# Performance work log

Hardware: AMD Instinct MI355X
Metric: run time of the kernel (lower is better)

The kernel has to match this reference:

```python
import jax, jax.numpy as jnp
import numpy as np

T = 5
EPS = 1e-05
G = 4      # num_groups
D = 64     # num_channels per group


def setup_inputs() -> dict:
    key = jax.random.key(0)
    X = jax.random.normal(key, (32, 256, 56, 56), dtype=jnp.float32)
    weight = jnp.ones((1, 256, 1, 1), dtype=jnp.float32)
    bias = jnp.zeros((1, 256, 1, 1), dtype=jnp.float32)
    return {"X": X, "weight": weight, "bias": bias}


def reference(X, weight, bias):
    N, C, H, W = X.shape
    # (N,C,H,W) -> (C,N,H,W) -> (g, d, m) with m = N*H*W
    x = X.transpose(1, 0, 2, 3).reshape(G, D, -1)
    m = x.shape[-1]
    mean = x.mean(-1, keepdims=True)                 # (g, d, 1)
    xc = x - mean
    I = jnp.eye(D, dtype=X.dtype)
    # Sigma = eps*I + xc xc^T / m     (g, d, d)
    Sigma = EPS * I + jnp.einsum('gdm,gem->gde', xc, xc) / m
    # trace normalization
    rTr = 1.0 / jnp.trace(Sigma, axis1=1, axis2=2)[:, None, None]  # (g,1,1)
    Sn = Sigma * rTr
    # Newton-Schulz iterations: P_{k+1} = 1.5 P_k - 0.5 P_k^3 Sn
    P = jnp.broadcast_to(I, (G, D, D))
    for _ in range(T):
        P = 1.5 * P - 0.5 * (P @ P @ P @ Sn)
    wm = P * jnp.sqrt(rTr)                           # whitening matrix (g,d,d)
    xn = wm @ xc                                     # (g, d, m)
    Xh = xn.reshape(C, N, H, W).transpose(1, 0, 2, 3)
    return Xh * weight + bias
```

## Files before the change

kernel.cpp:

```cpp
#include <hip/hip_runtime.h>
#include <math.h>

#define GROUPS 4
#define DCH    64
#define NBATCH 32
#define CTOT   256
#define HW     3136
#define CHW    (CTOT*HW)
#define MTOT   (NBATCH*HW)
#define EPSV   1e-5f

typedef __attribute__((ext_vector_type(8))) short bf16x8;
typedef __attribute__((ext_vector_type(4))) float f32x4;

__device__ __forceinline__ f32x4 mfma16(bf16x8 a, bf16x8 b, f32x4 c) {
    return __builtin_amdgcn_mfma_f32_16x16x32_bf16(a, b, c, 0, 0, 0);
}

__device__ __forceinline__ void split2(float x, short& h, short& l) {
    union { float f; unsigned u; } c; c.f = x;
    h = (short)(c.u >> 16);
    union { unsigned u; float f; } hm; hm.u = c.u & 0xFFFF0000u;
    union { float f; unsigned u; } lo; lo.f = x - hm.f;
    l = (short)(lo.u >> 16);
}

__device__ __forceinline__ void load_slab(const float* bp, float dst[16]) {
    float4 a0 = *reinterpret_cast<const float4*>(bp);
    float4 a1 = *reinterpret_cast<const float4*>(bp + 4);
    float4 b0 = *reinterpret_cast<const float4*>(bp + 32);
    float4 b1 = *reinterpret_cast<const float4*>(bp + 36);
    dst[0]=a0.x; dst[1]=a0.y; dst[2]=a0.z;  dst[3]=a0.w;
    dst[4]=a1.x; dst[5]=a1.y; dst[6]=a1.z;  dst[7]=a1.w;
    dst[8]=b0.x; dst[9]=b0.y; dst[10]=b0.z; dst[11]=b0.w;
    dst[12]=b1.x; dst[13]=b1.y; dst[14]=b1.z; dst[15]=b1.w;
}

template <int TPB>
__global__ __launch_bounds__(512) void k1_gram(const float* __restrict__ X,
                                               float* __restrict__ pGram,
                                               float* __restrict__ pSum)
{
    constexpr int KPB = MTOT / TPB;
    constexpr int NST = KPB / 128;
    const int pb   = blockIdx.x;
    const int g    = blockIdx.y;
    const int tid  = threadIdx.x;
    const int w    = tid >> 6;
    const int lane = tid & 63;
    const int tr   = w & 3;
    const int par  = w >> 2;
    const int lr   = lane & 15;
    const int q    = lane >> 4;

    __shared__ float smem[8192];
    __shared__ float rsum[2][64];

    f32x4 acc[4];
#pragma unroll
    for (int c = 0; c < 4; ++c) acc[c] = (f32x4)(0.f);
    float sumv = 0.f;

    const float* Xg  = X + (size_t)g * DCH * HW;
    const int    row = 16 * tr + lr;

    float xv[2][16];
    {
        const int kk = pb * KPB + par * 64;
        const int n  = kk / HW;
        const int s  = kk - n * HW;
        load_slab(Xg + (size_t)n * CHW + (size_t)row * HW + s + q * 8, xv[0]);
    }

#pragma unroll
    for (int t = 0; t < NST; ++t) {
        if (t + 1 < NST) {
            const int kk = pb * KPB + (t + 1) * 128 + par * 64;
            const int n  = kk / HW;
            const int s  = kk - n * HW;
            load_slab(Xg + (size_t)n * CHW + (size_t)row * HW + s + q * 8,
                      xv[(t + 1) & 1]);
        }
        bf16x8 ah[2], al[2];
#pragma unroll
        for (int ks = 0; ks < 2; ++ks) {
#pragma unroll
            for (int j = 0; j < 8; ++j) {
                float x = xv[t & 1][ks * 8 + j];
                sumv += x;
                short h, l; split2(x, h, l);
                ah[ks][j] = h; al[ks][j] = l;
            }
        }
#pragma unroll
        for (int ks = 0; ks < 2; ++ks) {
            *reinterpret_cast<bf16x8*>(&smem[(((par*4+tr)*2+ks)*2+0)*256 + lane*4]) = ah[ks];
            *reinterpret_cast<bf16x8*>(&smem[(((par*4+tr)*2+ks)*2+1)*256 + lane*4]) = al[ks];
        }
        __syncthreads();
#pragma unroll
        for (int c = 0; c < 4; ++c) {
#pragma unroll
            for (int ks = 0; ks < 2; ++ks) {
                bf16x8 bh = *reinterpret_cast<const bf16x8*>(
                    &smem[(((par*4+c)*2+ks)*2+0)*256 + lane*4]);
                bf16x8 bl = *reinterpret_cast<const bf16x8*>(
                    &smem[(((par*4+c)*2+ks)*2+1)*256 + lane*4]);
                acc[c] = mfma16(ah[ks], bh, acc[c]);
                acc[c] = mfma16(ah[ks], bl, acc[c]);
                acc[c] = mfma16(al[ks], bh, acc[c]);
            }
        }
        __syncthreads();
    }

    sumv += __shfl_xor(sumv, 16);
    sumv += __shfl_xor(sumv, 32);
    if (q == 0) rsum[par][row] = sumv;

#pragma unroll
    for (int c = 0; c < 4; ++c) {
#pragma unroll
        for (int r = 0; r < 4; ++r) {
            smem[par * 4096 + (16 * tr + 4 * q + r) * 64 + 16 * c + lr] = acc[c][r];
        }
    }
    __syncthreads();

    float* pg = pGram + ((size_t)g * TPB + pb) * 4096;
    for (int i = tid; i < 4096; i += 512) pg[i] = smem[i] + smem[4096 + i];
    if (tid < 64)
        pSum[((size_t)g * TPB + pb) * 64 + tid] = rsum[0][tid] + rsum[1][tid];
}

template <int S, int SLICE>
__global__ __launch_bounds__(256) void k2a1(const float* __restrict__ pGram,
                                            const float* __restrict__ pSum,
                                            float* __restrict__ pG2,
                                            float* __restrict__ pS2)
{
    const int cb  = blockIdx.x;
    const int g   = blockIdx.y;
    const int s   = blockIdx.z;
    const int tid = threadIdx.x;
    const int e = tid & 63, q = tid >> 6;
    __shared__ float red[4][64];
    __shared__ float red2[4][64];

    const float* pg = pGram + ((size_t)g * (S * SLICE) + s * SLICE + q) * 4096 + cb * 64 + e;
    float sum = 0.f;
#pragma unroll
    for (int i = 0; i < SLICE / 4; ++i)
        sum += pg[(size_t)i * 4 * 4096];
    red[q][e] = sum;
    if (cb == 0) {
        const float* ps = pSum + ((size_t)g * (S * SLICE) + s * SLICE + q) * 64 + e;
        float s2 = 0.f;
#pragma unroll
        for (int i = 0; i < SLICE / 4; ++i)
            s2 += ps[i * 4 * 64];
        red2[q][e] = s2;
    }
    __syncthreads();
    if (tid < 64) {
        pG2[((size_t)g * S + s) * 4096 + cb * 64 + tid] =
            red[0][tid] + red[1][tid] + red[2][tid] + red[3][tid];
        if (cb == 0)
            pS2[((size_t)g * S + s) * 64 + tid] =
                red2[0][tid] + red2[1][tid] + red2[2][tid] + red2[3][tid];
    }
}

template <int S>
__global__ __launch_bounds__(256) void k2a2(const float* __restrict__ pG2,
                                            const float* __restrict__ pS2,
                                            float* __restrict__ Gram,
                                            float* __restrict__ Mean)
{
    const int bx  = blockIdx.x;
    const int g   = blockIdx.y;
    const int tid = threadIdx.x;
    const int idx = bx * 256 + tid;

    float sum = 0.f;
#pragma unroll
    for (int s = 0; s < S; ++s)
        sum += pG2[((size_t)g * S + s) * 4096 + idx];
    Gram[g * 4096 + idx] = sum;

    if (bx == 0 && tid < 64) {
        float s2 = 0.f;
#pragma unroll
        for (int s = 0; s < S; ++s)
            s2 += pS2[((size_t)g * S + s) * 64 + tid];
        Mean[g * 64 + tid] = s2 * (1.0f / (float)MTOT);
    }
}

__device__ __forceinline__ void packrow2(const float* __restrict__ M, int row, int q,
                                         bf16x8& h0, bf16x8& l0,
                                         bf16x8& h1, bf16x8& l1)
{
    const float* p = M + row * 68 + 8 * q;
    float4 a0 = *reinterpret_cast<const float4*>(p);
    float4 a1 = *reinterpret_cast<const float4*>(p + 4);
    float4 b0 = *reinterpret_cast<const float4*>(p + 32);
    float4 b1 = *reinterpret_cast<const float4*>(p + 36);
    float e0[8] = {a0.x, a0.y, a0.z, a0.w, a1.x, a1.y, a1.z, a1.w};
    float e1[8] = {b0.x, b0.y, b0.z, b0.w, b1.x, b1.y, b1.z, b1.w};
#pragma unroll
    for (int j = 0; j < 8; ++j) {
        short h, l;
        split2(e0[j], h, l); h0[j] = h; l0[j] = l;
        split2(e1[j], h, l); h1[j] = h; l1[j] = l;
    }
}

__device__ __forceinline__ void mm_mfma(const float* __restrict__ A,
                                        const float* __restrict__ B,
                                        int w, int lr, int q, f32x4 acc[4])
{
    bf16x8 ah0, al0, ah1, al1;
    packrow2(A, 16 * w + lr, q, ah0, al0, ah1, al1);
#pragma unroll
    for (int c = 0; c < 4; ++c) {
        bf16x8 bh0, bl0, bh1, bl1;
        packrow2(B, 16 * c + lr, q, bh0, bl0, bh1, bl1);
        acc[c] = mfma16(ah0, bh0, acc[c]);
        acc[c] = mfma16(ah0, bl0, acc[c]);
        acc[c] = mfma16(al0, bh0, acc[c]);
        acc[c] = mfma16(ah1, bh1, acc[c]);
        acc[c] = mfma16(ah1, bl1, acc[c]);
        acc[c] = mfma16(al1, bh1, acc[c]);
    }
}

__global__ __launch_bounds__(256) void k2b_ns(const float* __restrict__ Gram,
                                              const float* __restrict__ Mean,
                                              const float* __restrict__ Wt,
                                              const float* __restrict__ Bs,
                                              float* __restrict__ Aout,
                                              float* __restrict__ Off)
{
    const int g   = blockIdx.x;
    const int tid = threadIdx.x;
    const int w = tid >> 6, lane = tid & 63, lr = lane & 15, q = lane >> 4;
    __shared__ float MP[64 * 68];
    __shared__ float MA[64 * 68];
    __shared__ float MB2[64 * 68];
    __shared__ float MS[64 * 68];
    __shared__ float lmean[64];
    __shared__ float redm[1024];
    __shared__ float rtr_s;

    if (tid < 64) lmean[tid] = Mean[g * 64 + tid];
    __syncthreads();
    for (int idx = tid; idx < 4096; idx += 256) {
        int d = idx >> 6, e = idx & 63;
        float v = Gram[g * 4096 + idx] * (1.0f / (float)MTOT) - lmean[d] * lmean[e];
        if (d == e) v += EPSV;
        MS[d * 68 + e] = v;
        MP[d * 68 + e] = (d == e) ? 1.f : 0.f;
    }
    __syncthreads();
    if (tid < 64) {
        float v = MS[tid * 68 + tid];
#pragma unroll
        for (int off = 32; off > 0; off >>= 1) v += __shfl_down(v, off);
        if (tid == 0) rtr_s = 1.f / v;
    }
    __syncthreads();
    const float rTr = rtr_s;
    for (int idx = tid; idx < 4096; idx += 256) {
        int d = idx >> 6, e = idx & 63;
        MS[d * 68 + e] *= rTr;
    }
    __syncthreads();

    const int row_o = 16 * w + 4 * q;
    for (int it = 0; it < 5; ++it) {
        f32x4 acc[4];
#pragma unroll
        for (int c = 0; c < 4; ++c) acc[c] = (f32x4)(0.f);
        mm_mfma(MP, MP, w, lr, q, acc);
#pragma unroll
        for (int c = 0; c < 4; ++c)
#pragma unroll
            for (int r = 0; r < 4; ++r)
                MA[(row_o + r) * 68 + 16 * c + lr] = acc[c][r];
        __syncthreads();

#pragma unroll
        for (int c = 0; c < 4; ++c) acc[c] = (f32x4)(0.f);
        mm_mfma(MA, MP, w, lr, q, acc);
#pragma unroll
        for (int c = 0; c < 4; ++c)
#pragma unroll
            for (int r = 0; r < 4; ++r)
                MB2[(row_o + r) * 68 + 16 * c + lr] = acc[c][r];
        __syncthreads();

#pragma unroll
        for (int c = 0; c < 4; ++c) acc[c] = (f32x4)(0.f);
        mm_mfma(MB2, MS, w, lr, q, acc);
#pragma unroll
        for (int c = 0; c < 4; ++c)
#pragma unroll
            for (int r = 0; r < 4; ++r) {
                int o = (row_o + r) * 68 + 16 * c + lr;
                MP[o] = 1.5f * MP[o] - 0.5f * acc[c][r];
            }
        __syncthreads();
    }

    const float sc = sqrtf(rTr);
    const int i0 = (tid >> 4) << 2, j0 = (tid & 15) << 2;
#pragma unroll
    for (int i = 0; i < 4; ++i) {
        int d = i0 + i;
        float wv = Wt[g * 64 + d] * sc;
        float4 v;
        v.x = MP[d * 68 + j0 + 0] * wv;
        v.y = MP[d * 68 + j0 + 1] * wv;
        v.z = MP[d * 68 + j0 + 2] * wv;
        v.w = MP[d * 68 + j0 + 3] * wv;
        *reinterpret_cast<float4*>(Aout + g * 4096 + (d << 6) + j0) = v;
        redm[(d << 4) + (tid & 15)] =
            v.x * lmean[j0] + v.y * lmean[j0 + 1] + v.z * lmean[j0 + 2] + v.w * lmean[j0 + 3];
    }
    __syncthreads();
    if (tid < 64) {
        float s = 0.f;
#pragma unroll
        for (int qq = 0; qq < 16; ++qq) s += redm[(tid << 4) + qq];
        Off[g * 64 + tid] = Bs[g * 64 + tid] - s;
    }
}

__global__ __launch_bounds__(256) void k3_apply(const float* __restrict__ X,
                                                const float* __restrict__ Aout,
                                                const float* __restrict__ Off,
                                                float* __restrict__ Y)
{
    const int c    = blockIdx.x;
    const int g    = blockIdx.y;
    const int tid  = threadIdx.x;
    const int w    = tid >> 6;
    const int lane = tid & 63;
    const int lr   = lane & 15;
    const int q    = lane >> 4;

    __shared__ float tile[4096];

    const int col0 = c * 64;
    const int n    = col0 / HW;
    const int s0   = col0 - n * HW;
    const float* Xg   = X + (size_t)g * DCH * HW;
    const float* base = Xg + (size_t)n * CHW + s0;

    float4 xr[4];
#pragma unroll
    for (int k = 0; k < 4; ++k) {
        int f = k * 256 + tid, r = f >> 4, gc = f & 15;
        xr[k] = *reinterpret_cast<const float4*>(base + (size_t)r * HW + gc * 4);
    }

    bf16x8 ah[2], al[2];
#pragma unroll
    for (int s = 0; s < 2; ++s) {
        const float* ap = Aout + g * 4096 + (16 * w + lr) * 64 + 32 * s + 8 * q;
        float4 v0 = *reinterpret_cast<const float4*>(ap);
        float4 v1 = *reinterpret_cast<const float4*>(ap + 4);
        float av[8] = {v0.x, v0.y, v0.z, v0.w, v1.x, v1.y, v1.z, v1.w};
#pragma unroll
        for (int j = 0; j < 8; ++j) {
            short h, l; split2(av[j], h, l);
            ah[s][j] = h; al[s][j] = l;
        }
    }
    float offv[4];
#pragma unroll
    for (int r = 0; r < 4; ++r) offv[r] = Off[g * 64 + 16 * w + 4 * q + r];

#pragma unroll
    for (int k = 0; k < 4; ++k) {
        int f = k * 256 + tid;
        *reinterpret_cast<float4*>(&tile[f * 4]) = xr[k];
    }
    __syncthreads();

    f32x4 accg[4];
#pragma unroll
    for (int j = 0; j < 4; ++j) accg[j] = (f32x4)(0.f);

#pragma unroll
    for (int ks = 0; ks < 2; ++ks) {
        bf16x8 bh[4], bl[4];
#pragma unroll
        for (int j8 = 0; j8 < 8; ++j8) {
            const int row = 32 * ks + 8 * q + j8;
            float4 v = *reinterpret_cast<const float4*>(&tile[row * 64 + lr * 4]);
            float vv[4] = {v.x, v.y, v.z, v.w};
#pragma unroll
            for (int jj = 0; jj < 4; ++jj) {
                short h, l; split2(vv[jj], h, l);
                bh[jj][j8] = h; bl[jj][j8] = l;
            }
        }
#pragma unroll
        for (int jj = 0; jj < 4; ++jj) {
            accg[jj] = mfma16(ah[ks], bh[jj], accg[jj]);
            accg[jj] = mfma16(ah[ks], bl[jj], accg[jj]);
            accg[jj] = mfma16(al[ks], bh[jj], accg[jj]);
        }
    }

    float* yp = Y + (size_t)g * DCH * HW + (size_t)n * CHW + s0 + 4 * lr;
#pragma unroll
    for (int r = 0; r < 4; ++r) {
        int row = 16 * w + 4 * q + r;
        float4 o;
        o.x = accg[0][r] + offv[r];
        o.y = accg[1][r] + offv[r];
        o.z = accg[2][r] + offv[r];
        o.w = accg[3][r] + offv[r];
        *reinterpret_cast<float4*>(yp + (size_t)row * HW) = o;
    }
}

extern "C" void kernel_launch(void* const* d_in, const int* in_sizes, int n_in,
                              void* d_out, int out_size, void* d_ws, size_t ws_size,
                              hipStream_t stream)
{
    const float* X  = (const float*)d_in[0];
    const float* Wt = (const float*)d_in[1];
    const float* Bs = (const float*)d_in[2];
    float* Y  = (float*)d_out;
    float* ws = (float*)d_ws;

    const size_t fixed = (size_t)4 * 4096 + 256 + (size_t)4 * 4096 + 256
                       + (size_t)4 * 7 * 4096 + (size_t)4 * 7 * 64;
    const size_t need392 = ((size_t)4 * 392 * 4096 + (size_t)4 * 392 * 64 + fixed) * sizeof(float);
    const int PBn = (ws_size >= need392) ? 392 : 196;

    float* pGram = ws;
    float* pSum  = pGram + (size_t)4 * PBn * 4096;
    float* Gram  = pSum  + (size_t)4 * PBn * 64;
    float* Mean  = Gram  + 4 * 4096;
    float* Aout  = Mean  + 256;
    float* Off   = Aout  + 4 * 4096;
    float* pG2   = Off   + 256;
    float* pS2   = pG2   + (size_t)4 * 7 * 4096;

    if (PBn == 392) {
        k1_gram<392><<<dim3(392, GROUPS), 512, 0, stream>>>(X, pGram, pSum);
        k2a1<7, 56><<<dim3(64, GROUPS, 7), 256, 0, stream>>>(pGram, pSum, pG2, pS2);
    } else {
        k1_gram<196><<<dim3(196, GROUPS), 512, 0, stream>>>(X, pGram, pSum);
        k2a1<7, 28><<<dim3(64, GROUPS, 7), 256, 0, stream>>>(pGram, pSum, pG2, pS2);
    }
    k2a2<7>   <<<dim3(16, GROUPS), 256, 0, stream>>>(pG2, pS2, Gram, Mean);
    k2b_ns    <<<dim3(GROUPS), 256, 0, stream>>>(Gram, Mean, Wt, Bs, Aout, Off);
    k3_apply  <<<dim3(1568, GROUPS), 256, 0, stream>>>(X, Aout, Off, Y);
}
```

Measured before the change: 85.73 us.

## Fuse final Gram reduction into NS kernel and shorten Newton-Schulz chain

Removes the separate final-reduction kernel by having the Newton-Schulz kernel sum the seven partial Gram/mean slices itself. Starts Newton-Schulz from the closed-form first iterate and computes P^2 and P*Sn in one phase, so each of the four remaining iterations needs two barrier phases instead of three. Also fixes the partial block count at 196, dropping the larger 392-block path, which halves k1's grid and may reduce its parallelism.

```diff
diff --git a/kernel.cpp b/kernel.cpp
--- a/kernel.cpp
+++ b/kernel.cpp
@@ -8,6 +8,7 @@
 #define HW     3136
 #define CHW    (CTOT*HW)
 #define MTOT   (NBATCH*HW)
+#define PB     196
 #define EPSV   1e-5f
 
 typedef __attribute__((ext_vector_type(8))) short bf16x8;
@@ -36,12 +37,11 @@
     dst[12]=b1.x; dst[13]=b1.y; dst[14]=b1.z; dst[15]=b1.w;
 }
 
-template <int TPB>
 __global__ __launch_bounds__(512) void k1_gram(const float* __restrict__ X,
                                                float* __restrict__ pGram,
                                                float* __restrict__ pSum)
 {
-    constexpr int KPB = MTOT / TPB;
+    constexpr int KPB = MTOT / PB;
     constexpr int NST = KPB / 128;
     const int pb   = blockIdx.x;
     const int g    = blockIdx.y;
@@ -127,18 +127,18 @@
     }
     __syncthreads();
 
-    float* pg = pGram + ((size_t)g * TPB + pb) * 4096;
+    float* pg = pGram + ((size_t)g * PB + pb) * 4096;
     for (int i = tid; i < 4096; i += 512) pg[i] = smem[i] + smem[4096 + i];
     if (tid < 64)
-        pSum[((size_t)g * TPB + pb) * 64 + tid] = rsum[0][tid] + rsum[1][tid];
-}
-
-template <int S, int SLICE>
+        pSum[((size_t)g * PB + pb) * 64 + tid] = rsum[0][tid] + rsum[1][tid];
+}
+
 __global__ __launch_bounds__(256) void k2a1(const float* __restrict__ pGram,
                                             const float* __restrict__ pSum,
                                             float* __restrict__ pG2,
                                             float* __restrict__ pS2)
 {
+    constexpr int SLICE = PB / 7;
     const int cb  = blockIdx.x;
     const int g   = blockIdx.y;
     const int s   = blockIdx.z;
@@ -147,14 +147,14 @@
     __shared__ float red[4][64];
     __shared__ float red2[4][64];
 
-    const float* pg = pGram + ((size_t)g * (S * SLICE) + s * SLICE + q) * 4096 + cb * 64 + e;
+    const float* pg = pGram + ((size_t)g * PB + s * SLICE + q) * 4096 + cb * 64 + e;
     float sum = 0.f;
 #pragma unroll
     for (int i = 0; i < SLICE / 4; ++i)
         sum += pg[(size_t)i * 4 * 4096];
     red[q][e] = sum;
     if (cb == 0) {
-        const float* ps = pSum + ((size_t)g * (S * SLICE) + s * SLICE + q) * 64 + e;
+        const float* ps = pSum + ((size_t)g * PB + s * SLICE + q) * 64 + e;
         float s2 = 0.f;
 #pragma unroll
         for (int i = 0; i < SLICE / 4; ++i)
@@ -163,37 +163,11 @@
     }
     __syncthreads();
     if (tid < 64) {
-        pG2[((size_t)g * S + s) * 4096 + cb * 64 + tid] =
+        pG2[((size_t)g * 7 + s) * 4096 + cb * 64 + tid] =
             red[0][tid] + red[1][tid] + red[2][tid] + red[3][tid];
         if (cb == 0)
-            pS2[((size_t)g * S + s) * 64 + tid] =
+            pS2[((size_t)g * 7 + s) * 64 + tid] =
                 red2[0][tid] + red2[1][tid] + red2[2][tid] + red2[3][tid];
-    }
-}
-
-template <int S>
-__global__ __launch_bounds__(256) void k2a2(const float* __restrict__ pG2,
-                                            const float* __restrict__ pS2,
-                                            float* __restrict__ Gram,
-                                            float* __restrict__ Mean)
-{
-    const int bx  = blockIdx.x;
-    const int g   = blockIdx.y;
-    const int tid = threadIdx.x;
-    const int idx = bx * 256 + tid;
-
-    float sum = 0.f;
-#pragma unroll
-    for (int s = 0; s < S; ++s)
-        sum += pG2[((size_t)g * S + s) * 4096 + idx];
-    Gram[g * 4096 + idx] = sum;
-
-    if (bx == 0 && tid < 64) {
-        float s2 = 0.f;
-#pragma unroll
-        for (int s = 0; s < S; ++s)
-            s2 += pS2[((size_t)g * S + s) * 64 + tid];
-        Mean[g * 64 + tid] = s2 * (1.0f / (float)MTOT);
     }
 }
 
@@ -216,27 +190,8 @@
     }
 }
 
-__device__ __forceinline__ void mm_mfma(const float* __restrict__ A,
-                                        const float* __restrict__ B,
-                                        int w, int lr, int q, f32x4 acc[4])
-{
-    bf16x8 ah0, al0, ah1, al1;
-    packrow2(A, 16 * w + lr, q, ah0, al0, ah1, al1);
-#pragma unroll
-    for (int c = 0; c < 4; ++c) {
-        bf16x8 bh0, bl0, bh1, bl1;
-        packrow2(B, 16 * c + lr, q, bh0, bl0, bh1, bl1);
-        acc[c] = mfma16(ah0, bh0, acc[c]);
-        acc[c] = mfma16(ah0, bl0, acc[c]);
-        acc[c] = mfma16(al0, bh0, acc[c]);
-        acc[c] = mfma16(ah1, bh1, acc[c]);
-        acc[c] = mfma16(ah1, bl1, acc[c]);
-        acc[c] = mfma16(al1, bh1, acc[c]);
-    }
-}
-
-__global__ __launch_bounds__(256) void k2b_ns(const float* __restrict__ Gram,
-                                              const float* __restrict__ Mean,
+__global__ __launch_bounds__(256) void k2b_ns(const float* __restrict__ pG2,
+                                              const float* __restrict__ pS2,
                                               const float* __restrict__ Wt,
                                               const float* __restrict__ Bs,
                                               float* __restrict__ Aout,
@@ -253,14 +208,21 @@
     __shared__ float redm[1024];
     __shared__ float rtr_s;
 
-    if (tid < 64) lmean[tid] = Mean[g * 64 + tid];
+    if (tid < 64) {
+        float s2 = 0.f;
+#pragma unroll
+        for (int s = 0; s < 7; ++s) s2 += pS2[((size_t)g * 7 + s) * 64 + tid];
+        lmean[tid] = s2 * (1.0f / (float)MTOT);
+    }
     __syncthreads();
     for (int idx = tid; idx < 4096; idx += 256) {
         int d = idx >> 6, e = idx & 63;
-        float v = Gram[g * 4096 + idx] * (1.0f / (float)MTOT) - lmean[d] * lmean[e];
+        float sum = 0.f;
+#pragma unroll
+        for (int s = 0; s < 7; ++s) sum += pG2[((size_t)g * 7 + s) * 4096 + idx];
+        float v = sum * (1.0f / (float)MTOT) - lmean[d] * lmean[e];
         if (d == e) v += EPSV;
         MS[d * 68 + e] = v;
-        MP[d * 68 + e] = (d == e) ? 1.f : 0.f;
     }
     __syncthreads();
     if (tid < 64) {
@@ -273,36 +235,63 @@
     const float rTr = rtr_s;
     for (int idx = tid; idx < 4096; idx += 256) {
         int d = idx >> 6, e = idx & 63;
-        MS[d * 68 + e] *= rTr;
+        float sv = MS[d * 68 + e] * rTr;
+        MS[d * 68 + e] = sv;
+        MP[d * 68 + e] = ((d == e) ? 1.5f : 0.f) - 0.5f * sv;
     }
     __syncthreads();
 
     const int row_o = 16 * w + 4 * q;
-    for (int it = 0; it < 5; ++it) {
+    for (int it = 0; it < 4; ++it) {
+        f32x4 a2[4], aS[4];
+#pragma unroll
+        for (int c = 0; c < 4; ++c) { a2[c] = (f32x4)(0.f); aS[c] = (f32x4)(0.f); }
+        bf16x8 pah0, pal0, pah1, pal1;
+        packrow2(MP, 16 * w + lr, q, pah0, pal0, pah1, pal1);
+#pragma unroll
+        for (int c = 0; c < 4; ++c) {
+            bf16x8 bh0, bl0, bh1, bl1;
+            packrow2(MP, 16 * c + lr, q, bh0, bl0, bh1, bl1);
+            a2[c] = mfma16(pah0, bh0, a2[c]);
+            a2[c] = mfma16(pah0, bl0, a2[c]);
+            a2[c] = mfma16(pal0, bh0, a2[c]);
+            a2[c] = mfma16(pah1, bh1, a2[c]);
+            a2[c] = mfma16(pah1, bl1, a2[c]);
+            a2[c] = mfma16(pal1, bh1, a2[c]);
+            bf16x8 sh0, sl0, sh1, sl1;
+            packrow2(MS, 16 * c + lr, q, sh0, sl0, sh1, sl1);
+            aS[c] = mfma16(pah0, sh0, aS[c]);
+            aS[c] = mfma16(pah0, sl0, aS[c]);
+            aS[c] = mfma16(pal0, sh0, aS[c]);
+            aS[c] = mfma16(pah1, sh1, aS[c]);
+            aS[c] = mfma16(pah1, sl1, aS[c]);
+            aS[c] = mfma16(pal1, sh1, aS[c]);
+        }
+#pragma unroll
+        for (int c = 0; c < 4; ++c)
+#pragma unroll
+            for (int r = 0; r < 4; ++r) {
+                MA [(row_o + r) * 68 + 16 * c + lr] = a2[c][r];
+                MB2[(row_o + r) * 68 + 16 * c + lr] = aS[c][r];
+            }
+        __syncthreads();
+
         f32x4 acc[4];
 #pragma unroll
         for (int c = 0; c < 4; ++c) acc[c] = (f32x4)(0.f);
-        mm_mfma(MP, MP, w, lr, q, acc);
-#pragma unroll
-        for (int c = 0; c < 4; ++c)
-#pragma unroll
-            for (int r = 0; r < 4; ++r)
-                MA[(row_o + r) * 68 + 16 * c + lr] = acc[c][r];
-        __syncthreads();
-
-#pragma unroll
-        for (int c = 0; c < 4; ++c) acc[c] = (f32x4)(0.f);
-        mm_mfma(MA, MP, w, lr, q, acc);
-#pragma unroll
-        for (int c = 0; c < 4; ++c)
-#pragma unroll
-            for (int r = 0; r < 4; ++r)
-                MB2[(row_o + r) * 68 + 16 * c + lr] = acc[c][r];
-        __syncthreads();
-
-#pragma unroll
-        for (int c = 0; c < 4; ++c) acc[c] = (f32x4)(0.f);
-        mm_mfma(MB2, MS, w, lr, q, acc);
+        bf16x8 qah0, qal0, qah1, qal1;
+        packrow2(MA, 16 * w + lr, q, qah0, qal0, qah1, qal1);
+#pragma unroll
+        for (int c = 0; c < 4; ++c) {
+            bf16x8 bh0, bl0, bh1, bl1;
+            packrow2(MB2, 16 * c + lr, q, bh0, bl0, bh1, bl1);
+            acc[c] = mfma16(qah0, bh0, acc[c]);
+            acc[c] = mfma16(qah0, bl0, acc[c]);
+            acc[c] = mfma16(qal0, bh0, acc[c]);
+            acc[c] = mfma16(qah1, bh1, acc[c]);
+            acc[c] = mfma16(qah1, bl1, acc[c]);
+            acc[c] = mfma16(qal1, bh1, acc[c]);
+        }
 #pragma unroll
         for (int c = 0; c < 4; ++c)
 #pragma unroll
@@ -438,28 +427,15 @@
     float* Y  = (float*)d_out;
     float* ws = (float*)d_ws;
 
-    const size_t fixed = (size_t)4 * 4096 + 256 + (size_t)4 * 4096 + 256
-                       + (size_t)4 * 7 * 4096 + (size_t)4 * 7 * 64;
-    const size_t need392 = ((size_t)4 * 392 * 4096 + (size_t)4 * 392 * 64 + fixed) * sizeof(float);
-    const int PBn = (ws_size >= need392) ? 392 : 196;
-
     float* pGram = ws;
-    float* pSum  = pGram + (size_t)4 * PBn * 4096;
-    float* Gram  = pSum  + (size_t)4 * PBn * 64;
-    float* Mean  = Gram  + 4 * 4096;
-    float* Aout  = Mean  + 256;
+    float* pSum  = pGram + (size_t)4 * PB * 4096;
+    float* pG2   = pSum  + (size_t)4 * PB * 64;
+    float* pS2   = pG2   + (size_t)4 * 7 * 4096;
+    float* Aout  = pS2   + (size_t)4 * 7 * 64;
     float* Off   = Aout  + 4 * 4096;
-    float* pG2   = Off   + 256;
-    float* pS2   = pG2   + (size_t)4 * 7 * 4096;
-
-    if (PBn == 392) {
-        k1_gram<392><<<dim3(392, GROUPS), 512, 0, stream>>>(X, pGram, pSum);
-        k2a1<7, 56><<<dim3(64, GROUPS, 7), 256, 0, stream>>>(pGram, pSum, pG2, pS2);
-    } else {
-        k1_gram<196><<<dim3(196, GROUPS), 512, 0, stream>>>(X, pGram, pSum);
-        k2a1<7, 28><<<dim3(64, GROUPS, 7), 256, 0, stream>>>(pGram, pSum, pG2, pS2);
-    }
-    k2a2<7>   <<<dim3(16, GROUPS), 256, 0, stream>>>(pG2, pS2, Gram, Mean);
-    k2b_ns    <<<dim3(GROUPS), 256, 0, stream>>>(Gram, Mean, Wt, Bs, Aout, Off);
-    k3_apply  <<<dim3(1568, GROUPS), 256, 0, stream>>>(X, Aout, Off, Y);
-}
+
+    k1_gram <<<dim3(PB, GROUPS), 512, 0, stream>>>(X, pGram, pSum);
+    k2a1    <<<dim3(64, GROUPS, 7), 256, 0, stream>>>(pGram, pSum, pG2, pS2);
+    k2b_ns  <<<dim3(GROUPS), 256, 0, stream>>>(pG2, pS2, Wt, Bs, Aout, Off);
+    k3_apply<<<dim3(1568, GROUPS), 256, 0, stream>>>(X, Aout, Off, Y);
+}
```

Result: faster. 81.84 us (-4.5%).
